# Performance work log

Hardware: AMD Instinct MI355X
Metric: run time of the kernel (lower is better)

The kernel has to match this reference:

```python
import jax, jax.numpy as jnp
import numpy as np
from jax import lax

ROI = 3
NMS_SIZE = 1024
NMS_THRESH = 0.8
X_MIN = -40.0   # area_extents x
Z_MAX = 70.0    # area_extents z


def crop_and_resize(fmap, boxes, crop):
    """tf.image.crop_and_resize on a single-channel single-image map.
    fmap: [H, W]; boxes: [N, 4] normalized [y1, x1, y2, x2]. Returns [N, crop, crop]."""
    H, W = fmap.shape
    dt = fmap.dtype
    y1, x1, y2, x2 = boxes[:, 0], boxes[:, 1], boxes[:, 2], boxes[:, 3]
    t = jnp.arange(crop, dtype=dt) / (crop - 1)
    ys = (y1[:, None] + (y2 - y1)[:, None] * t) * (H - 1)   # [N, crop]
    xs = (x1[:, None] + (x2 - x1)[:, None] * t) * (W - 1)   # [N, crop]
    y0 = jnp.floor(ys); x0 = jnp.floor(xs)
    wy = (ys - y0)[:, :, None]; wx = (xs - x0)[:, None, :]
    y0i = jnp.clip(y0, 0, H - 1).astype(jnp.int32)
    y1i = jnp.clip(y0 + 1, 0, H - 1).astype(jnp.int32)
    x0i = jnp.clip(x0, 0, W - 1).astype(jnp.int32)
    x1i = jnp.clip(x0 + 1, 0, W - 1).astype(jnp.int32)
    g = lambda yi, xi: fmap[yi[:, :, None], xi[:, None, :]]  # [N, crop, crop]
    v = (g(y0i, x0i) * (1 - wy) * (1 - wx) + g(y0i, x1i) * (1 - wy) * wx
         + g(y1i, x0i) * wy * (1 - wx) + g(y1i, x1i) * wy * wx)
    valid = (((ys >= 0) & (ys <= H - 1))[:, :, None]
             & ((xs >= 0) & (xs <= W - 1))[:, None, :])
    return jnp.where(valid, v, jnp.zeros((), dt))


def nms(boxes, scores, thresh, max_out):
    """Greedy NMS (tf.image.non_max_suppression). boxes [N,4] = [y1,x1,y2,x2].
    Returns max_out indices (fixed shape; trailing slots padded with suppressed boxes)."""
    N = boxes.shape[0]
    order = jnp.argsort(-scores)
    b = boxes[order]
    area = (b[:, 2] - b[:, 0]) * (b[:, 3] - b[:, 1])
    tl = jnp.maximum(b[:, None, :2], b[None, :, :2])
    br = jnp.minimum(b[:, None, 2:], b[None, :, 2:])
    wh = jnp.maximum(br - tl, 0.0)
    inter = wh[..., 0] * wh[..., 1]
    iou = inter / (area[:, None] + area[None, :] - inter + 1e-9)
    over = iou > thresh  # [N, N] bool

    def body(supp, xs):
        row, i = xs
        keep_i = ~supp[i]
        supp = supp | (keep_i & row)
        return supp, keep_i

    _, keep = lax.scan(body, jnp.zeros(N, bool), (over, jnp.arange(N)))
    ar = jnp.arange(N)
    sel = jnp.argsort(jnp.where(keep, ar, N + ar))[:max_out]
    return lax.stop_gradient(order[sel])


def setup_inputs() -> dict:
    key = jax.random.key(0)
    ks = jax.random.split(key, 16)
    N, C = 8192, 32
    f32 = jnp.float32
    img_map = jax.random.normal(ks[0], (1, 360, 1200, C), f32)
    bev_map = jax.random.normal(ks[1], (1, 704, 800, C), f32)

    def make_boxes(k):
        k1, k2, k3, k4 = jax.random.split(k, 4)
        x1 = jax.random.uniform(k1, (N,), f32) * 0.8
        y1 = jax.random.uniform(k2, (N,), f32) * 0.8
        w = 0.02 + 0.15 * jax.random.uniform(k3, (N,), f32)
        h = 0.02 + 0.15 * jax.random.uniform(k4, (N,), f32)
        zero = jnp.zeros((N,), f32)
        # columns: [batch_idx, x1, y1, x2, y2]
        return jnp.stack([zero, x1, y1, jnp.minimum(x1 + w, 1.0),
                          jnp.minimum(y1 + h, 1.0)], axis=1)

    anchors_img = make_boxes(ks[2])
    anchors_bev = make_boxes(ks[3])
    u = jax.random.uniform(ks[4], (N, 6), f32)
    filtered_anchors = jnp.stack([
        -35.0 + 70.0 * u[:, 0],   # x in area extents
        -3.0 + 4.0 * u[:, 1],     # y
        2.0 + 66.0 * u[:, 2],     # z
        1.5 + 3.0 * u[:, 3],      # dx
        1.2 + 0.8 * u[:, 4],      # dy
        1.5 + 3.0 * u[:, 5],      # dz
    ], axis=1)
    s = 0.02
    F = ROI * ROI  # fused ROI is [N,3,3,1] -> 9 features
    return {
        'img_map': img_map, 'bev_map': bev_map,
        'anchors_img': anchors_img, 'anchors_bev': anchors_bev,
        'filtered_anchors': filtered_anchors,
        'w_img': jax.random.normal(ks[5], (C, 1), f32) * s, 'b_img': jnp.zeros((1,), f32),
        'w_bev': jax.random.normal(ks[6], (C, 1), f32) * s, 'b_bev': jnp.zeros((1,), f32),
        'w_obj': jax.random.normal(ks[7], (F, 2), f32) * s, 'b_obj': jnp.zeros((2,), f32),
        'w_off': jax.random.normal(ks[8], (F, 6), f32) * s, 'b_off': jnp.zeros((6,), f32),
        'img_mask': jnp.ones((), f32), 'bev_mask': jnp.ones((), f32),
    }


def reference(img_map, bev_map, anchors_img, anchors_bev, filtered_anchors,
              w_img, b_img, w_bev, b_bev, w_obj, b_obj, w_off, b_off,
              img_mask, bev_mask):
    # 1x1 conv + relu to single-channel score maps
    x1 = jax.nn.relu(jnp.einsum('bhwc,co->bhwo', img_map, w_img) + b_img)
    x2 = jax.nn.relu(jnp.einsum('bhwc,co->bhwo', bev_map, w_bev) + b_bev)
    # gather([2,1,4,3]) -> [y1, x1, y2, x2]
    boxes_img = anchors_img[:, jnp.array([2, 1, 4, 3])]
    boxes_bev = anchors_bev[:, jnp.array([2, 1, 4, 3])]
    roi_rgb = crop_and_resize((img_mask * x1)[0, :, :, 0], boxes_img, ROI)
    roi_bev = crop_and_resize((bev_mask * x2)[0, :, :, 0], boxes_bev, ROI)
    # Fusion: mean of paths, normalized by number of active paths
    fused = (roi_rgb + roi_bev) / (img_mask + bev_mask)
    feat = fused.reshape(fused.shape[0], -1)  # [N, 9]
    objectness = feat @ w_obj + b_obj         # [N, 2]
    offsets = feat @ w_off + b_off            # [N, 6]
    # offset_predictions_to_anchors (AVOD decode): centers shifted by t*dim, dims = dim*exp(t)
    a_xyz, a_dim = filtered_anchors[:, :3], filtered_anchors[:, 3:]
    reg_anchors = jnp.concatenate(
        [a_xyz + offsets[:, :3] * a_dim, a_dim * jnp.exp(offsets[:, 3:])], axis=1)
    # project_to_bev (normalize=False): [z1, x1, z2, x2] in metric BEV frame
    cx, cz = reg_anchors[:, 0], reg_anchors[:, 2]
    dx, dz = reg_anchors[:, 3], reg_anchors[:, 5]
    bx1 = cx - dx / 2 - X_MIN
    bx2 = cx + dx / 2 - X_MIN
    bz1 = Z_MAX - (cz + dz / 2)
    bz2 = Z_MAX - (cz - dz / 2)
    bev_boxes = jnp.stack([bz1, bx1, bz2, bx2], axis=1)
    scores = jax.nn.softmax(objectness, axis=1)[:, 1]
    top_idx = nms(bev_boxes, scores, NMS_THRESH, NMS_SIZE)
    return reg_anchors[top_idx], objectness[top_idx]
```

## Files before the change

### kernel.cpp

```cpp
#include <hip/hip_runtime.h>
#include <math.h>

#define NBOX 8192
#define NW   128
#define NB   4096
#define NBW  64
#define NF   9
#define MAXOUT 1024
#define IMG_H 360
#define IMG_W 1200
#define BEV_H 704
#define BEV_W 800

__device__ float g_feat[NBOX * NF];
__device__ float g_score[NBOX];
__device__ float g_reg[NBOX * 6];
__device__ float g_obj[NBOX * 2];
__device__ float g_bev[NBOX * 4];
__device__ float g_sbev[NBOX * 4];
__device__ float g_sarea[NBOX];
__device__ int   g_rank[NBOX];
__device__ int   g_order[NBOX];
__device__ unsigned long long g_mask[(size_t)NB * NW];
__device__ unsigned long long g_rownz[NW];

__device__ __forceinline__ float expf_cr(float x) { return (float)exp((double)x); }

__device__ __forceinline__ float conv_relu_m(const float* __restrict__ map,
                                             const float* __restrict__ w,
                                             float bias, float mask,
                                             int y, int x, int W) {
  const float* p = map + ((size_t)y * W + x) * 32;
  float L0 = 0.0f, L1 = 0.0f, L2 = 0.0f, L3 = 0.0f;
#pragma unroll
  for (int c = 0; c < 32; c += 4) {
    L0 = __fadd_rn(L0, __fmul_rn(p[c + 0], w[c + 0]));
    L1 = __fadd_rn(L1, __fmul_rn(p[c + 1], w[c + 1]));
    L2 = __fadd_rn(L2, __fmul_rn(p[c + 2], w[c + 2]));
    L3 = __fadd_rn(L3, __fmul_rn(p[c + 3], w[c + 3]));
  }
  float A = __fadd_rn(L0, L1);
  float B = __fadd_rn(L2, L3);
  float conv = __fadd_rn(A, B);
  conv = __fadd_rn(conv, bias);
  float r = fmaxf(conv, 0.0f);
  return __fmul_rn(mask, r);
}

__global__ __launch_bounds__(256) void roi_feat_kernel(
    const float* __restrict__ img_map, const float* __restrict__ bev_map,
    const float* __restrict__ anc_img, const float* __restrict__ anc_bev,
    const float* __restrict__ w_img, const float* __restrict__ b_img,
    const float* __restrict__ w_bev, const float* __restrict__ b_bev,
    const float* __restrict__ img_mask, const float* __restrict__ bev_mask) {
  __shared__ float sg[32][12];
  int tid = threadIdx.x;
  int grp = tid >> 3, sub = tid & 7;
  int gidx = blockIdx.x * 32 + grp;
  int box = gidx / NF, s = gidx % NF;
  int gy = s / 3, gx = s % 3;
  bool isImg = (sub < 4);

  float mi = img_mask[0], mb = bev_mask[0];
  const float* A   = (isImg ? anc_img : anc_bev) + (size_t)box * 5;
  const float* map = isImg ? img_map : bev_map;
  const float* wv  = isImg ? w_img : w_bev;
  float bias = isImg ? b_img[0] : b_bev[0];
  float mk   = isImg ? mi : mb;
  int H = isImg ? IMG_H : BEV_H;
  int W = isImg ? IMG_W : BEV_W;
  float y1 = A[2], x1 = A[1], y2 = A[4], x2 = A[3];

  const float tt0 = 0.0f, tt1 = 0.5f, tt2 = 1.0f;
  float ty = (gy == 0) ? tt0 : (gy == 1 ? tt1 : tt2);
  float tx = (gx == 0) ? tt0 : (gx == 1 ? tt1 : tt2);
  float ys = __fmul_rn(__fadd_rn(y1, __fmul_rn(__fsub_rn(y2, y1), ty)), (float)(H - 1));
  float xs = __fmul_rn(__fadd_rn(x1, __fmul_rn(__fsub_rn(x2, x1), tx)), (float)(W - 1));
  bool valid = (ys >= 0.0f) && (ys <= (float)(H - 1)) && (xs >= 0.0f) && (xs <= (float)(W - 1));
  float y0 = floorf(ys), x0 = floorf(xs);
  float wy = __fsub_rn(ys, y0);
  float wx = __fsub_rn(xs, x0);
  int y0i = (int)fminf(fmaxf(y0, 0.0f), (float)(H - 1));
  int y1i = (int)fminf(fmaxf(__fadd_rn(y0, 1.0f), 0.0f), (float)(H - 1));
  int x0i = (int)fminf(fmaxf(x0, 0.0f), (float)(W - 1));
  int x1i = (int)fminf(fmaxf(__fadd_rn(x0, 1.0f), 0.0f), (float)(W - 1));

  int py = (sub & 2) ? y1i : y0i;
  int px = (sub & 1) ? x1i : x0i;
  sg[grp][sub] = conv_relu_m(map, wv, bias, mk, py, px, W);
  if (sub == 4) {
    sg[grp][8]  = wy;
    sg[grp][9]  = wx;
    sg[grp][10] = valid ? 1.0f : 0.0f;
  }
  __syncthreads();
  if (sub == 0) {
    float vi = 0.0f;
    if (valid) {
      float a = __fsub_rn(1.0f, wy);
      float b = __fsub_rn(1.0f, wx);
      float t1 = __fmul_rn(__fmul_rn(sg[grp][0], a), b);
      float t2 = __fmul_rn(__fmul_rn(sg[grp][1], a), wx);
      float t3 = __fmul_rn(__fmul_rn(sg[grp][2], wy), b);
      float t4 = __fmul_rn(__fmul_rn(sg[grp][3], wy), wx);
      vi = __fadd_rn(__fadd_rn(__fadd_rn(t1, t2), t3), t4);
    }
    float vb = 0.0f;
    if (sg[grp][10] != 0.0f) {
      float wyB = sg[grp][8], wxB = sg[grp][9];
      float a = __fsub_rn(1.0f, wyB);
      float b = __fsub_rn(1.0f, wxB);
      float t1 = __fmul_rn(__fmul_rn(sg[grp][4], a), b);
      float t2 = __fmul_rn(__fmul_rn(sg[grp][5], a), wxB);
      float t3 = __fmul_rn(__fmul_rn(sg[grp][6], wyB), b);
      float t4 = __fmul_rn(__fmul_rn(sg[grp][7], wyB), wxB);
      vb = __fadd_rn(__fadd_rn(__fadd_rn(t1, t2), t3), t4);
    }
    g_feat[gidx] = __fdiv_rn(__fadd_rn(vi, vb), __fadd_rn(mi, mb));
  }
}

__global__ __launch_bounds__(256) void head_kernel(
    const float* __restrict__ fa,
    const float* __restrict__ w_obj, const float* __restrict__ b_obj,
    const float* __restrict__ w_off, const float* __restrict__ b_off) {
  int i = blockIdx.x * 256 + threadIdx.x;
  if (i >= NBOX) return;
  g_rank[i] = 0;
  if (i < NW) g_rownz[i] = 0ull;
  float f[NF];
#pragma unroll
  for (int k = 0; k < NF; ++k) f[k] = g_feat[(size_t)i * NF + k];

  float o0 = 0.0f, o1 = 0.0f;
#pragma unroll
  for (int k = 0; k < NF; ++k) {
    o0 = fmaf(f[k], w_obj[k * 2 + 0], o0);
    o1 = fmaf(f[k], w_obj[k * 2 + 1], o1);
  }
  o0 = __fadd_rn(o0, b_obj[0]);
  o1 = __fadd_rn(o1, b_obj[1]);

  float off[6];
#pragma unroll
  for (int m = 0; m < 6; ++m) {
    float s = 0.0f;
#pragma unroll
    for (int k = 0; k < NF; ++k) s = fmaf(f[k], w_off[k * 6 + m], s);
    off[m] = __fadd_rn(s, b_off[m]);
  }

  float reg[6];
#pragma unroll
  for (int k = 0; k < 3; ++k)
    reg[k] = __fadd_rn(fa[i * 6 + k], __fmul_rn(off[k], fa[i * 6 + 3 + k]));
#pragma unroll
  for (int k = 0; k < 3; ++k)
    reg[3 + k] = __fmul_rn(fa[i * 6 + 3 + k], expf_cr(off[3 + k]));

#pragma unroll
  for (int k = 0; k < 6; ++k) g_reg[i * 6 + k] = reg[k];
  g_obj[i * 2 + 0] = o0;
  g_obj[i * 2 + 1] = o1;

  float m  = fmaxf(o0, o1);
  float d0 = __fsub_rn(o0, m);
  float d1 = __fsub_rn(o1, m);
  float e0 = expf_cr(d0);
  float e1 = expf_cr(d1);
  float sm = __fadd_rn(e0, e1);
  g_score[i] = __fdiv_rn(e1, sm);

  float cx = reg[0], cz = reg[2], dx = reg[3], dz = reg[5];
  float dxh = __fdiv_rn(dx, 2.0f);
  float dzh = __fdiv_rn(dz, 2.0f);
  g_bev[i * 4 + 0] = __fsub_rn(70.0f, __fadd_rn(cz, dzh));
  g_bev[i * 4 + 1] = __fsub_rn(__fsub_rn(cx, dxh), -40.0f);
  g_bev[i * 4 + 2] = __fsub_rn(70.0f, __fsub_rn(cz, dzh));
  g_bev[i * 4 + 3] = __fsub_rn(__fadd_rn(cx, dxh), -40.0f);
}

__global__ __launch_bounds__(256) void rank_kernel() {
  __shared__ float kj[256];
  int tid = threadIdx.x;
  int i = blockIdx.x * 256 + tid;
  int jbase = blockIdx.y * 256;
  kj[tid] = g_score[jbase + tid];
  float ki = g_score[i];
  __syncthreads();
  int cnt = 0;
#pragma unroll 8
  for (int k = 0; k < 256; ++k) {
    float v = kj[k];
    int j = jbase + k;
    cnt += (v > ki) || (v == ki && j < i);
  }
  atomicAdd(&g_rank[i], cnt);
}

__global__ __launch_bounds__(256) void scatter_kernel() {
  int i = blockIdx.x * 256 + threadIdx.x;
  if (i >= NBOX) return;
  int r = g_rank[i];
  g_order[r] = i;
  float b0 = g_bev[i * 4 + 0], b1 = g_bev[i * 4 + 1];
  float b2 = g_bev[i * 4 + 2], b3 = g_bev[i * 4 + 3];
  g_sbev[r * 4 + 0] = b0; g_sbev[r * 4 + 1] = b1;
  g_sbev[r * 4 + 2] = b2; g_sbev[r * 4 + 3] = b3;
  g_sarea[r] = __fmul_rn(__fsub_rn(b2, b0), __fsub_rn(b3, b1));
}

__global__ __launch_bounds__(256) void mask_kernel() {
  __shared__ float sb[4][64 * 5];
  int tid = threadIdx.x;
  int wv = tid >> 6, lane = tid & 63;
  int t = blockIdx.x * 4 + wv;
  int r = t >> 6, c = t & 63;
  int i = r * 64 + lane;
  if (c < r) {
    g_mask[(size_t)i * NW + c] = 0ull;
    return;
  }
  {
    int j = c * 64 + lane;
    sb[wv][lane * 5 + 0] = g_sbev[j * 4 + 0];
    sb[wv][lane * 5 + 1] = g_sbev[j * 4 + 1];
    sb[wv][lane * 5 + 2] = g_sbev[j * 4 + 2];
    sb[wv][lane * 5 + 3] = g_sbev[j * 4 + 3];
    sb[wv][lane * 5 + 4] = g_sarea[j];
  }
  float y1 = g_sbev[i * 4 + 0], x1 = g_sbev[i * 4 + 1];
  float y2 = g_sbev[i * 4 + 2], x2 = g_sbev[i * 4 + 3];
  float ai = g_sarea[i];
  unsigned long long bits = 0ull;
  int jbase = c * 64;
  for (int k = 0; k < 64; ++k) {
    int j = jbase + k;
    float by1 = sb[wv][k * 5 + 0], bx1 = sb[wv][k * 5 + 1];
    float by2 = sb[wv][k * 5 + 2], bx2 = sb[wv][k * 5 + 3], aj = sb[wv][k * 5 + 4];
    float ih = fmaxf(__fsub_rn(fminf(y2, by2), fmaxf(y1, by1)), 0.0f);
    float iw = fmaxf(__fsub_rn(fminf(x2, bx2), fmaxf(x1, bx1)), 0.0f);
    float inter = __fmul_rn(ih, iw);
    float t1 = __fadd_rn(ai, aj);
    float t2 = __fsub_rn(t1, inter);
    float t3 = __fadd_rn(t2, 1e-9f);
    float iou = __fdiv_rn(inter, t3);
    bool over = (j > i) && (iou > 0.8f);
    bits |= over ? (1ull << k) : 0ull;
  }
  g_mask[(size_t)i * NW + c] = bits;
  if (bits) atomicOr(&g_rownz[i >> 6], 1ull << (i & 63));
}

#define LOAD_C(X, T0)                                                   \
  _Pragma("unroll")                                                     \
  for (int k = 0; k < 8; ++k) {                                         \
    int tt = (T0) + k;                                                  \
    X[k] = (tt < total) ? g_mask[(size_t)pos_s[tt] * NW + tid] : 0ull;  \
  }

#define PROC_C(X, T0)                                                   \
  _Pragma("unroll")                                                     \
  for (int k = 0; k < 8; ++k) {                                         \
    int tt = (T0) + k;                                                  \
    int p  = pos_s[tt];                                                 \
    int w  = p >> 6, bb = p & 63;                                       \
    unsigned long long cw = __shfl(remv, w, 64);                        \
    if (tt < total && !((cw >> bb) & 1ull)) remv |= X[k];               \
  }

__global__ __launch_bounds__(256) void scan_select_kernel(float* __restrict__ out) {
  __shared__ unsigned short pos_s[NB + 64];
  __shared__ unsigned long long kept_s[NBW];
  __shared__ int pk[NW], ps[NW];
  __shared__ int totK, total_s;
  __shared__ int tidx[MAXOUT];
  int tid = threadIdx.x;

  if (tid < 64) {
    unsigned long long r = g_rownz[tid];
    int pc = __popcll(r);
    int s = pc;
#pragma unroll
    for (int d = 1; d < 64; d <<= 1) {
      int t = __shfl_up(s, d, 64);
      if (tid >= d) s += t;
    }
    int total = __shfl(s, 63, 64);
    unsigned long long m = r; int idx = s - pc;
    while (m) { int b = __builtin_ctzll(m); m &= m - 1;
                pos_s[idx++] = (unsigned short)(tid * 64 + b); }
    pos_s[total + tid] = 0;
    if (tid == 0) total_s = total;

    unsigned long long remv = 0ull;
    unsigned long long A[8], B[8], C[8];
    LOAD_C(A, 0)
    LOAD_C(B, 8)
    LOAD_C(C, 16)
    for (int t0 = 0; t0 < total; t0 += 24) {
      PROC_C(A, t0)
      LOAD_C(A, t0 + 24)
      PROC_C(B, t0 + 8)
      LOAD_C(B, t0 + 32)
      PROC_C(C, t0 + 16)
      LOAD_C(C, t0 + 40)
    }
    kept_s[tid] = ~remv;
  }
  __syncthreads();
  if (tid < NW) {
    int kc = (tid < NBW) ? __popcll(kept_s[tid]) : 0;
    pk[tid] = kc;
    ps[tid] = 64 - kc;
  }
  __syncthreads();
  if (tid == 0) {
    int s = 0;
    for (int w = 0; w < NW; ++w) { int t = pk[w]; pk[w] = s; s += t; }
    totK = s;
    s = 0;
    for (int w = 0; w < NW; ++w) { int t = ps[w]; ps[w] = s; s += t; }
  }
  __syncthreads();
  if (tid < NW) {
    unsigned long long kw = (tid < NBW) ? kept_s[tid] : 0ull;
    int rk = pk[tid], rs = totK + ps[tid];
    for (int b = 0; b < 64; ++b) {
      int pos = tid * 64 + b;
      if ((kw >> b) & 1ull) {
        if (rk < MAXOUT) tidx[rk] = g_order[pos];
        rk++;
      } else {
        if (rs < MAXOUT) tidx[rs] = g_order[pos];
        rs++;
      }
    }
  }
  __syncthreads();
  for (int k = tid; k < MAXOUT; k += 256) {
    int ti = tidx[k];
#pragma unroll
    for (int m = 0; m < 6; ++m) out[k * 6 + m] = g_reg[ti * 6 + m];
    out[MAXOUT * 6 + k * 2 + 0] = g_obj[ti * 2 + 0];
    out[MAXOUT * 6 + k * 2 + 1] = g_obj[ti * 2 + 1];
  }
}

extern "C" void kernel_launch(void* const* d_in, const int* in_sizes, int n_in,
                              void* d_out, int out_size, void* d_ws, size_t ws_size,
                              hipStream_t stream) {
  const float* img_map  = (const float*)d_in[0];
  const float* bev_map  = (const float*)d_in[1];
  const float* anc_img  = (const float*)d_in[2];
  const float* anc_bev  = (const float*)d_in[3];
  const float* fa       = (const float*)d_in[4];
  const float* w_img    = (const float*)d_in[5];
  const float* b_img    = (const float*)d_in[6];
  const float* w_bev    = (const float*)d_in[7];
  const float* b_bev    = (const float*)d_in[8];
  const float* w_obj    = (const float*)d_in[9];
  const float* b_obj    = (const float*)d_in[10];
  const float* w_off    = (const float*)d_in[11];
  const float* b_off    = (const float*)d_in[12];
  const float* img_mask = (const float*)d_in[13];
  const float* bev_mask = (const float*)d_in[14];
  float* out = (float*)d_out;

  roi_feat_kernel<<<dim3(2304), dim3(256), 0, stream>>>(
      img_map, bev_map, anc_img, anc_bev, w_img, b_img, w_bev, b_bev, img_mask, bev_mask);
  head_kernel<<<dim3(32), dim3(256), 0, stream>>>(fa, w_obj, b_obj, w_off, b_off);
  rank_kernel<<<dim3(32, 32), dim3(256), 0, stream>>>();
  scatter_kernel<<<dim3(32), dim3(256), 0, stream>>>();
  mask_kernel<<<dim3(1024), dim3(256), 0, stream>>>();
  scan_select_kernel<<<dim3(1), dim3(256), 0, stream>>>(out);
}
```

Before: 74.83 us.

## Fuse six kernels into three using last-block completion counters

Result: slower. 229.8 us (+207.1%).

```diff
diff --git a/kernel.cpp b/kernel.cpp
--- a/kernel.cpp
+++ b/kernel.cpp
@@ -12,7 +12,6 @@
 #define BEV_H 704
 #define BEV_W 800
 
-__device__ float g_feat[NBOX * NF];
 __device__ float g_score[NBOX];
 __device__ float g_reg[NBOX * 6];
 __device__ float g_obj[NBOX * 2];
@@ -23,6 +22,8 @@
 __device__ int   g_order[NBOX];
 __device__ unsigned long long g_mask[(size_t)NB * NW];
 __device__ unsigned long long g_rownz[NW];
+__device__ int   rank_done;
+__device__ int   mask_done;
 
 __device__ __forceinline__ float expf_cr(float x) { return (float)exp((double)x); }
 
@@ -47,19 +48,29 @@
   return __fmul_rn(mask, r);
 }
 
-__global__ __launch_bounds__(256) void roi_feat_kernel(
+__global__ __launch_bounds__(576) void roi_head_kernel(
     const float* __restrict__ img_map, const float* __restrict__ bev_map,
     const float* __restrict__ anc_img, const float* __restrict__ anc_bev,
+    const float* __restrict__ fa,
     const float* __restrict__ w_img, const float* __restrict__ b_img,
     const float* __restrict__ w_bev, const float* __restrict__ b_bev,
+    const float* __restrict__ w_obj, const float* __restrict__ b_obj,
+    const float* __restrict__ w_off, const float* __restrict__ b_off,
     const float* __restrict__ img_mask, const float* __restrict__ bev_mask) {
-  __shared__ float sg[32][12];
+  __shared__ float sg[72][12];
+  __shared__ float feat_s[72];
   int tid = threadIdx.x;
   int grp = tid >> 3, sub = tid & 7;
-  int gidx = blockIdx.x * 32 + grp;
+  int gidx = blockIdx.x * 72 + grp;
   int box = gidx / NF, s = gidx % NF;
   int gy = s / 3, gx = s % 3;
   bool isImg = (sub < 4);
+
+  if (tid < 8) g_rank[blockIdx.x * 8 + tid] = 0;
+  if (blockIdx.x == 0) {
+    if (tid < NW) g_rownz[tid] = 0ull;
+    if (tid == 0) { rank_done = 0; mask_done = 0; }
+  }
 
   float mi = img_mask[0], mb = bev_mask[0];
   const float* A   = (isImg ? anc_img : anc_bev) + (size_t)box * 5;
@@ -116,147 +127,102 @@
       float t4 = __fmul_rn(__fmul_rn(sg[grp][7], wyB), wxB);
       vb = __fadd_rn(__fadd_rn(__fadd_rn(t1, t2), t3), t4);
     }
-    g_feat[gidx] = __fdiv_rn(__fadd_rn(vi, vb), __fadd_rn(mi, mb));
-  }
-}
-
-__global__ __launch_bounds__(256) void head_kernel(
-    const float* __restrict__ fa,
-    const float* __restrict__ w_obj, const float* __restrict__ b_obj,
-    const float* __restrict__ w_off, const float* __restrict__ b_off) {
-  int i = blockIdx.x * 256 + threadIdx.x;
-  if (i >= NBOX) return;
-  g_rank[i] = 0;
-  if (i < NW) g_rownz[i] = 0ull;
-  float f[NF];
-#pragma unroll
-  for (int k = 0; k < NF; ++k) f[k] = g_feat[(size_t)i * NF + k];
-
-  float o0 = 0.0f, o1 = 0.0f;
-#pragma unroll
-  for (int k = 0; k < NF; ++k) {
-    o0 = fmaf(f[k], w_obj[k * 2 + 0], o0);
-    o1 = fmaf(f[k], w_obj[k * 2 + 1], o1);
-  }
-  o0 = __fadd_rn(o0, b_obj[0]);
-  o1 = __fadd_rn(o1, b_obj[1]);
-
-  float off[6];
-#pragma unroll
-  for (int m = 0; m < 6; ++m) {
-    float s = 0.0f;
-#pragma unroll
-    for (int k = 0; k < NF; ++k) s = fmaf(f[k], w_off[k * 6 + m], s);
-    off[m] = __fadd_rn(s, b_off[m]);
-  }
-
-  float reg[6];
-#pragma unroll
-  for (int k = 0; k < 3; ++k)
-    reg[k] = __fadd_rn(fa[i * 6 + k], __fmul_rn(off[k], fa[i * 6 + 3 + k]));
-#pragma unroll
-  for (int k = 0; k < 3; ++k)
-    reg[3 + k] = __fmul_rn(fa[i * 6 + 3 + k], expf_cr(off[3 + k]));
-
-#pragma unroll
-  for (int k = 0; k < 6; ++k) g_reg[i * 6 + k] = reg[k];
-  g_obj[i * 2 + 0] = o0;
-  g_obj[i * 2 + 1] = o1;
-
-  float m  = fmaxf(o0, o1);
-  float d0 = __fsub_rn(o0, m);
-  float d1 = __fsub_rn(o1, m);
-  float e0 = expf_cr(d0);
-  float e1 = expf_cr(d1);
-  float sm = __fadd_rn(e0, e1);
-  g_score[i] = __fdiv_rn(e1, sm);
-
-  float cx = reg[0], cz = reg[2], dx = reg[3], dz = reg[5];
-  float dxh = __fdiv_rn(dx, 2.0f);
-  float dzh = __fdiv_rn(dz, 2.0f);
-  g_bev[i * 4 + 0] = __fsub_rn(70.0f, __fadd_rn(cz, dzh));
-  g_bev[i * 4 + 1] = __fsub_rn(__fsub_rn(cx, dxh), -40.0f);
-  g_bev[i * 4 + 2] = __fsub_rn(70.0f, __fsub_rn(cz, dzh));
-  g_bev[i * 4 + 3] = __fsub_rn(__fadd_rn(cx, dxh), -40.0f);
-}
-
-__global__ __launch_bounds__(256) void rank_kernel() {
-  __shared__ float kj[256];
+    feat_s[grp] = __fdiv_rn(__fadd_rn(vi, vb), __fadd_rn(mi, mb));
+  }
+  __syncthreads();
+  if (tid < 8) {
+    int i = blockIdx.x * 8 + tid;
+    float f[NF];
+#pragma unroll
+    for (int k = 0; k < NF; ++k) f[k] = feat_s[tid * NF + k];
+
+    float o0 = 0.0f, o1 = 0.0f;
+#pragma unroll
+    for (int k = 0; k < NF; ++k) {
+      o0 = fmaf(f[k], w_obj[k * 2 + 0], o0);
+      o1 = fmaf(f[k], w_obj[k * 2 + 1], o1);
+    }
+    o0 = __fadd_rn(o0, b_obj[0]);
+    o1 = __fadd_rn(o1, b_obj[1]);
+
+    float off[6];
+#pragma unroll
+    for (int m = 0; m < 6; ++m) {
+      float sv = 0.0f;
+#pragma unroll
+      for (int k = 0; k < NF; ++k) sv = fmaf(f[k], w_off[k * 6 + m], sv);
+      off[m] = __fadd_rn(sv, b_off[m]);
+    }
+
+    float reg[6];
+#pragma unroll
+    for (int k = 0; k < 3; ++k)
+      reg[k] = __fadd_rn(fa[i * 6 + k], __fmul_rn(off[k], fa[i * 6 + 3 + k]));
+#pragma unroll
+    for (int k = 0; k < 3; ++k)
+      reg[3 + k] = __fmul_rn(fa[i * 6 + 3 + k], expf_cr(off[3 + k]));
+
+#pragma unroll
+    for (int k = 0; k < 6; ++k) g_reg[i * 6 + k] = reg[k];
+    g_obj[i * 2 + 0] = o0;
+    g_obj[i * 2 + 1] = o1;
+
+    float m  = fmaxf(o0, o1);
+    float d0 = __fsub_rn(o0, m);
+    float d1 = __fsub_rn(o1, m);
+    float e0 = expf_cr(d0);
+    float e1 = expf_cr(d1);
+    float sm = __fadd_rn(e0, e1);
+    g_score[i] = __fdiv_rn(e1, sm);
+
+    float cx = reg[0], cz = reg[2], dx = reg[3], dz = reg[5];
+    float dxh = __fdiv_rn(dx, 2.0f);
+    float dzh = __fdiv_rn(dz, 2.0f);
+    g_bev[i * 4 + 0] = __fsub_rn(70.0f, __fadd_rn(cz, dzh));
+    g_bev[i * 4 + 1] = __fsub_rn(__fsub_rn(cx, dxh), -40.0f);
+    g_bev[i * 4 + 2] = __fsub_rn(70.0f, __fsub_rn(cz, dzh));
+    g_bev[i * 4 + 3] = __fsub_rn(__fadd_rn(cx, dxh), -40.0f);
+  }
+}
+
+__global__ __launch_bounds__(256) void rank_scatter_kernel() {
+  __shared__ float kj[1024];
+  __shared__ int last_s;
   int tid = threadIdx.x;
   int i = blockIdx.x * 256 + tid;
-  int jbase = blockIdx.y * 256;
-  kj[tid] = g_score[jbase + tid];
+  int jbase = blockIdx.y * 1024;
+  for (int k = tid; k < 1024; k += 256) kj[k] = g_score[jbase + k];
   float ki = g_score[i];
   __syncthreads();
   int cnt = 0;
 #pragma unroll 8
-  for (int k = 0; k < 256; ++k) {
+  for (int k = 0; k < 1024; ++k) {
     float v = kj[k];
     int j = jbase + k;
     cnt += (v > ki) || (v == ki && j < i);
   }
   atomicAdd(&g_rank[i], cnt);
-}
-
-__global__ __launch_bounds__(256) void scatter_kernel() {
-  int i = blockIdx.x * 256 + threadIdx.x;
-  if (i >= NBOX) return;
-  int r = g_rank[i];
-  g_order[r] = i;
-  float b0 = g_bev[i * 4 + 0], b1 = g_bev[i * 4 + 1];
-  float b2 = g_bev[i * 4 + 2], b3 = g_bev[i * 4 + 3];
-  g_sbev[r * 4 + 0] = b0; g_sbev[r * 4 + 1] = b1;
-  g_sbev[r * 4 + 2] = b2; g_sbev[r * 4 + 3] = b3;
-  g_sarea[r] = __fmul_rn(__fsub_rn(b2, b0), __fsub_rn(b3, b1));
-}
-
-__global__ __launch_bounds__(256) void mask_kernel() {
-  __shared__ float sb[4][64 * 5];
-  int tid = threadIdx.x;
-  int wv = tid >> 6, lane = tid & 63;
-  int t = blockIdx.x * 4 + wv;
-  int r = t >> 6, c = t & 63;
-  int i = r * 64 + lane;
-  if (c < r) {
-    g_mask[(size_t)i * NW + c] = 0ull;
-    return;
-  }
-  {
-    int j = c * 64 + lane;
-    sb[wv][lane * 5 + 0] = g_sbev[j * 4 + 0];
-    sb[wv][lane * 5 + 1] = g_sbev[j * 4 + 1];
-    sb[wv][lane * 5 + 2] = g_sbev[j * 4 + 2];
-    sb[wv][lane * 5 + 3] = g_sbev[j * 4 + 3];
-    sb[wv][lane * 5 + 4] = g_sarea[j];
-  }
-  float y1 = g_sbev[i * 4 + 0], x1 = g_sbev[i * 4 + 1];
-  float y2 = g_sbev[i * 4 + 2], x2 = g_sbev[i * 4 + 3];
-  float ai = g_sarea[i];
-  unsigned long long bits = 0ull;
-  int jbase = c * 64;
-  for (int k = 0; k < 64; ++k) {
-    int j = jbase + k;
-    float by1 = sb[wv][k * 5 + 0], bx1 = sb[wv][k * 5 + 1];
-    float by2 = sb[wv][k * 5 + 2], bx2 = sb[wv][k * 5 + 3], aj = sb[wv][k * 5 + 4];
-    float ih = fmaxf(__fsub_rn(fminf(y2, by2), fmaxf(y1, by1)), 0.0f);
-    float iw = fmaxf(__fsub_rn(fminf(x2, bx2), fmaxf(x1, bx1)), 0.0f);
-    float inter = __fmul_rn(ih, iw);
-    float t1 = __fadd_rn(ai, aj);
-    float t2 = __fsub_rn(t1, inter);
-    float t3 = __fadd_rn(t2, 1e-9f);
-    float iou = __fdiv_rn(inter, t3);
-    bool over = (j > i) && (iou > 0.8f);
-    bits |= over ? (1ull << k) : 0ull;
-  }
-  g_mask[(size_t)i * NW + c] = bits;
-  if (bits) atomicOr(&g_rownz[i >> 6], 1ull << (i & 63));
+  __threadfence();
+  if (tid == 0) last_s = (atomicAdd(&rank_done, 1) == 32 * 8 - 1);
+  __syncthreads();
+  if (!last_s) return;
+  for (int p = tid; p < NBOX; p += 256) {
+    int r = atomicAdd(&g_rank[p], 0);
+    g_order[r] = p;
+    float b0 = g_bev[p * 4 + 0], b1 = g_bev[p * 4 + 1];
+    float b2 = g_bev[p * 4 + 2], b3 = g_bev[p * 4 + 3];
+    g_sbev[r * 4 + 0] = b0; g_sbev[r * 4 + 1] = b1;
+    g_sbev[r * 4 + 2] = b2; g_sbev[r * 4 + 3] = b3;
+    g_sarea[r] = __fmul_rn(__fsub_rn(b2, b0), __fsub_rn(b3, b1));
+  }
 }
 
 #define LOAD_C(X, T0)                                                   \
   _Pragma("unroll")                                                     \
   for (int k = 0; k < 8; ++k) {                                         \
     int tt = (T0) + k;                                                  \
-    X[k] = (tt < total) ? g_mask[(size_t)pos_s[tt] * NW + tid] : 0ull;  \
+    X[k] = (tt < total) ?                                               \
+      atomicOr(&g_mask[(size_t)pos_s[tt] * NW + tid], 0ull) : 0ull;     \
   }
 
 #define PROC_C(X, T0)                                                   \
@@ -269,16 +235,61 @@
     if (tt < total && !((cw >> bb) & 1ull)) remv |= X[k];               \
   }
 
-__global__ __launch_bounds__(256) void scan_select_kernel(float* __restrict__ out) {
+__global__ __launch_bounds__(256) void mask_scan_kernel(float* __restrict__ out) {
+  __shared__ float sb[4][64 * 5];
+  __shared__ int last_s;
   __shared__ unsigned short pos_s[NB + 64];
   __shared__ unsigned long long kept_s[NBW];
   __shared__ int pk[NW], ps[NW];
-  __shared__ int totK, total_s;
+  __shared__ int totK;
   __shared__ int tidx[MAXOUT];
   int tid = threadIdx.x;
+  int wv = tid >> 6, lane = tid & 63;
+  {
+    int t = blockIdx.x * 4 + wv;
+    int r = t >> 6, c = t & 63;
+    int i = r * 64 + lane;
+    if (c < r) {
+      g_mask[(size_t)i * NW + c] = 0ull;
+    } else {
+      int j = c * 64 + lane;
+      sb[wv][lane * 5 + 0] = g_sbev[j * 4 + 0];
+      sb[wv][lane * 5 + 1] = g_sbev[j * 4 + 1];
+      sb[wv][lane * 5 + 2] = g_sbev[j * 4 + 2];
+      sb[wv][lane * 5 + 3] = g_sbev[j * 4 + 3];
+      sb[wv][lane * 5 + 4] = g_sarea[j];
+      float y1 = g_sbev[i * 4 + 0], x1 = g_sbev[i * 4 + 1];
+      float y2 = g_sbev[i * 4 + 2], x2 = g_sbev[i * 4 + 3];
+      float ai = g_sarea[i];
+      unsigned long long bits = 0ull;
+      int jbase = c * 64;
+      for (int k = 0; k < 64; ++k) {
+        int j2 = jbase + k;
+        float by1 = sb[wv][k * 5 + 0], bx1 = sb[wv][k * 5 + 1];
+        float by2 = sb[wv][k * 5 + 2], bx2 = sb[wv][k * 5 + 3], aj = sb[wv][k * 5 + 4];
+        float ih = fmaxf(__fsub_rn(fminf(y2, by2), fmaxf(y1, by1)), 0.0f);
+        float iw = fmaxf(__fsub_rn(fminf(x2, bx2), fmaxf(x1, bx1)), 0.0f);
+        float inter = __fmul_rn(ih, iw);
+        float t1 = __fadd_rn(ai, aj);
+        float t2 = __fsub_rn(t1, inter);
+        float t3 = __fadd_rn(t2, 1e-9f);
+        float iou = __fdiv_rn(inter, t3);
+        bool over = (j2 > i) && (iou > 0.8f);
+        bits |= over ? (1ull << k) : 0ull;
+      }
+      g_mask[(size_t)i * NW + c] = bits;
+      if (bits) atomicOr(&g_rownz[i >> 6], 1ull << (i & 63));
+    }
+  }
+  __threadfence();
+  __syncthreads();
+  if (tid == 0) last_s = (atomicAdd(&mask_done, 1) == 1023);
+  __syncthreads();
+  if (!last_s) return;
+  __threadfence();
 
   if (tid < 64) {
-    unsigned long long r = g_rownz[tid];
+    unsigned long long r = atomicOr(&g_rownz[tid], 0ull);
     int pc = __popcll(r);
     int s = pc;
 #pragma unroll
@@ -291,7 +302,6 @@
     while (m) { int b = __builtin_ctzll(m); m &= m - 1;
                 pos_s[idx++] = (unsigned short)(tid * 64 + b); }
     pos_s[total + tid] = 0;
-    if (tid == 0) total_s = total;
 
     unsigned long long remv = 0ull;
     unsigned long long A[8], B[8], C[8];
@@ -367,11 +377,9 @@
   const float* bev_mask = (const float*)d_in[14];
   float* out = (float*)d_out;
 
-  roi_feat_kernel<<<dim3(2304), dim3(256), 0, stream>>>(
-      img_map, bev_map, anc_img, anc_bev, w_img, b_img, w_bev, b_bev, img_mask, bev_mask);
-  head_kernel<<<dim3(32), dim3(256), 0, stream>>>(fa, w_obj, b_obj, w_off, b_off);
-  rank_kernel<<<dim3(32, 32), dim3(256), 0, stream>>>();
-  scatter_kernel<<<dim3(32), dim3(256), 0, stream>>>();
-  mask_kernel<<<dim3(1024), dim3(256), 0, stream>>>();
-  scan_select_kernel<<<dim3(1), dim3(256), 0, stream>>>(out);
-}
+  roi_head_kernel<<<dim3(1024), dim3(576), 0, stream>>>(
+      img_map, bev_map, anc_img, anc_bev, fa, w_img, b_img, w_bev, b_bev,
+      w_obj, b_obj, w_off, b_off, img_mask, bev_mask);
+  rank_scatter_kernel<<<dim3(32, 8), dim3(256), 0, stream>>>();
+  mask_scan_kernel<<<dim3(1024), dim3(256), 0, stream>>>(out);
+}
```
